# Kernel optimization log

Measured on AMD Instinct MI355X. Metric: run time of the kernel, lower is better.

## Reference

```python
import jax, jax.numpy as jnp
import numpy as np

DECAY = 0.99
EPS = 1e-5
COMMIT_COST = 0.25
VQ_COST = 1.0
COUNTER = 1  # first EMA step (hidden buffers are zero-initialized)


def setup_inputs() -> dict:
    key = jax.random.key(0)
    k1, k2 = jax.random.split(key)
    B, D, T, K = 64, 128, 2048, 1024
    x = jax.random.normal(k1, (B, D, T), dtype=jnp.float32)
    # xavier_uniform for [K, D]
    limit = float(np.sqrt(6.0 / (K + D)))
    embeddings = jax.random.uniform(k2, (K, D), minval=-limit, maxval=limit, dtype=jnp.float32)
    ema_dw_hidden = jnp.zeros((K, D), dtype=jnp.float32)
    ema_cluster_hidden = jnp.zeros((K,), dtype=jnp.float32)
    return {"x": x, "embeddings": embeddings,
            "ema_dw_hidden": ema_dw_hidden, "ema_cluster_hidden": ema_cluster_hidden}


def reference(x, embeddings, ema_dw_hidden, ema_cluster_hidden):
    K, D = embeddings.shape
    xt = jnp.transpose(x, (0, 2, 1))          # [B, T, D]
    flat = xt.reshape(-1, D)                  # [N, D]
    dist = (jnp.sum(flat * flat, axis=1, keepdims=True)
            + jnp.sum(embeddings * embeddings, axis=1)
            - 2.0 * flat @ embeddings.T)      # [N, K]
    idx = jnp.argmin(dist, axis=1)            # [N]
    quantized = embeddings[idx].reshape(xt.shape)  # [B, T, D]

    # --- EMA codebook update (no grad; pure stats) ---
    counts = jax.ops.segment_sum(jnp.ones_like(idx, dtype=jnp.float32), idx, num_segments=K)  # [K]
    hid_cs = ema_cluster_hidden - (ema_cluster_hidden - counts) * (1.0 - DECAY)
    avg_cs = hid_cs / (1.0 - DECAY ** COUNTER)
    n = jnp.sum(avg_cs)
    cs = (avg_cs + EPS) / (n + K * EPS) * n   # Laplace-smoothed cluster size
    dw = jax.ops.segment_sum(flat, idx, num_segments=K)  # [K, D] == encodings.T @ flat
    hid_dw = ema_dw_hidden - (ema_dw_hidden - dw) * (1.0 - DECAY)
    avg_dw = hid_dw / (1.0 - DECAY ** COUNTER)
    new_embeddings = avg_dw / cs[:, None]

    # --- losses + straight-through estimator ---
    sg = jax.lax.stop_gradient
    loss_commit = COMMIT_COST * jnp.mean((xt - sg(quantized)) ** 2)
    loss_vq = VQ_COST * jnp.mean((sg(xt) - quantized) ** 2)
    q_st = xt + sg(quantized - xt)
    out = jnp.transpose(q_st, (0, 2, 1))      # [B, D, T]
    return (out, loss_commit, loss_vq, idx, new_embeddings)
```

## Files before the change

### kernel.cpp

```cpp
#include <hip/hip_runtime.h>

#define NB 64
#define ND 128
#define NT 2048
#define NK 1024
#define NN (NB*NT)
#define DTSTRIDE (ND*NT)

typedef __attribute__((ext_vector_type(8))) short bf16x8;
typedef __attribute__((ext_vector_type(4))) float floatx4;

#define WS_ET    0
#define WS_SSX   131072
#define WS_SSE   262144
#define WS_DW    263168
#define WS_CS    394240
#define WS_CNT   395264
#define WS_IDX   396288
#define WS_LOSS  527360
#define WS_OFFS  527364
#define WS_CUR   528388
#define WS_LIST  529412
#define WS_XT    660736
#define WS_EB    17437952

#define O_OUT 0
#define O_LC  16777216
#define O_LV  16777217
#define O_IDX 16777218
#define O_NE  16908290

#define GLL16(g, l) __builtin_amdgcn_global_load_lds( \
    (const __attribute__((address_space(1))) unsigned int*)(g), \
    (__attribute__((address_space(3))) unsigned int*)(l), 16, 0, 0)

__device__ inline void split1(float v, unsigned short &a, unsigned short &b,
                              unsigned short &c) {
    unsigned int u = __float_as_uint(v);
    a = (unsigned short)(u >> 16);
    float f1 = __uint_as_float(u & 0xffff0000u);
    float r = v - f1;
    unsigned int ur = __float_as_uint(r);
    b = (unsigned short)(ur >> 16);
    float f2 = __uint_as_float(ur & 0xffff0000u);
    float r2 = r - f2;
    c = (unsigned short)(__float_as_uint(r2) >> 16);
}

__device__ inline void split2(float va, float vb, unsigned int &p1,
                              unsigned int &p2, unsigned int &p3) {
    unsigned int ua = __float_as_uint(va), ub = __float_as_uint(vb);
    p1 = (ua >> 16) | (ub & 0xffff0000u);
    float fa = __uint_as_float(ua & 0xffff0000u);
    float fb = __uint_as_float(ub & 0xffff0000u);
    float ra = va - fa, rb = vb - fb;
    unsigned int ura = __float_as_uint(ra), urb = __float_as_uint(rb);
    p2 = (ura >> 16) | (urb & 0xffff0000u);
    float f2a = __uint_as_float(ura & 0xffff0000u);
    float f2b = __uint_as_float(urb & 0xffff0000u);
    float r2a = ra - f2a, r2b = rb - f2b;
    p3 = (__float_as_uint(r2a) >> 16) | (__float_as_uint(r2b) & 0xffff0000u);
}

__global__ void prep_e(const float* __restrict__ emb, float* __restrict__ ET,
                       float* __restrict__ sse, unsigned short* __restrict__ eb1,
                       unsigned short* __restrict__ eb2, unsigned short* __restrict__ eb3) {
    int tid = threadIdx.x;
    int k   = blockIdx.x * 16 + (tid >> 4);
    int l   = tid & 15;
    float ss = 0.f;
    #pragma unroll
    for (int it = 0; it < 2; ++it) {
        int d0 = l * 4 + it * 64;
        float4 v = *(const float4*)(emb + k * ND + d0);
        ET[(d0+0)*NK + k] = v.x;
        ET[(d0+1)*NK + k] = v.y;
        ET[(d0+2)*NK + k] = v.z;
        ET[(d0+3)*NK + k] = v.w;
        ss = fmaf(v.x, v.x, ss); ss = fmaf(v.y, v.y, ss);
        ss = fmaf(v.z, v.z, ss); ss = fmaf(v.w, v.w, ss);
        int dc  = (l >> 3) + it * 2;
        int d5  = d0 & 31;
        int qb  = (d5 >> 3) & 3;
        int sl  = qb ^ ((k >> 1) & 3);
        int off = (dc * NK + k) * 32 + (sl << 3) + (d5 & 7);
        ushort4 a, b, c;
        split1(v.x, a.x, b.x, c.x);
        split1(v.y, a.y, b.y, c.y);
        split1(v.z, a.z, b.z, c.z);
        split1(v.w, a.w, b.w, c.w);
        *(ushort4*)(eb1 + off) = a;
        *(ushort4*)(eb2 + off) = b;
        *(ushort4*)(eb3 + off) = c;
    }
    for (int m = 1; m <= 8; m <<= 1) ss += __shfl_xor(ss, m);
    if (l == 0) sse[k] = ss;
}

__global__ void transpose_x(const float* __restrict__ x, float* __restrict__ xt,
                            float* __restrict__ ssx) {
    __shared__ float tile[128][33];
    int tid = threadIdx.x;
    int b   = blockIdx.x >> 6;
    int t0  = (blockIdx.x & 63) << 5;
    int tl  = tid & 31;
    int dg  = tid >> 5;
    const float* xp = x + b * DTSTRIDE + t0 + tl;
    #pragma unroll
    for (int p = 0; p < 16; ++p) {
        int d = p * 8 + dg;
        tile[d][tl] = xp[d * NT];
    }
    __syncthreads();
    float* xtp = xt + (size_t)(b * NT + t0) * ND;
    #pragma unroll
    for (int c = 0; c < 4; ++c) {
        int d = c * 32 + (tid & 31);
        #pragma unroll
        for (int p = 0; p < 4; ++p) {
            int tr = p * 8 + (tid >> 5);
            xtp[tr * ND + d] = tile[d][tr];
        }
    }
    if (tid < 32) {
        float ss = 0.f;
        #pragma unroll 8
        for (int d = 0; d < ND; ++d) {
            float v = tile[d][tid];
            ss = fmaf(v, v, ss);
        }
        ssx[b * NT + t0 + tid] = ss;
    }
}

__device__ __forceinline__ void stage_eb(int ktp, int dcp, int bufidx, int w, int lane,
        unsigned short* smem, const unsigned short* eb1,
        const unsigned short* eb2, const unsigned short* eb3) {
    int goff = (dcp << 15) + (ktp << 12);
    int bufo = bufidx * 12288;
    #pragma unroll
    for (int i = 0; i < 2; ++i) {
        int ch = (w << 1) + i;
        int so = goff + (ch << 9) + (lane << 3);
        GLL16(eb1 + so, &smem[bufo + 0*4096 + (ch << 9)]);
        GLL16(eb2 + so, &smem[bufo + 1*4096 + (ch << 9)]);
        GLL16(eb3 + so, &smem[bufo + 2*4096 + (ch << 9)]);
    }
}

__device__ __forceinline__ int m3(int v) { return v >= 3 ? v - 3 : v; }

__launch_bounds__(256, 2)
__global__ void gemm_argmin_mfma(const float* __restrict__ xt,
                                 const unsigned short* __restrict__ eb1,
                                 const unsigned short* __restrict__ eb2,
                                 const unsigned short* __restrict__ eb3,
                                 const float* __restrict__ ssx, const float* __restrict__ sse,
                                 float* __restrict__ out, int* __restrict__ idxi,
                                 int* __restrict__ counts, float* __restrict__ loss) {
    __shared__ unsigned short smem[38912];
    int tid = threadIdx.x;
    int b   = blockIdx.x >> 4;
    int t0  = (blockIdx.x & 15) << 7;
    int n0  = b * NT + t0;

    int lane = tid & 63;
    int w    = tid >> 6;
    int c    = lane & 15;
    int q    = lane >> 4;
    int slot = q ^ ((c >> 1) & 3);

    stage_eb(0, 0, 0, w, lane, smem, eb1, eb2, eb3);

    float* ssef = (float*)&smem[36864];
    ((float4*)ssef)[tid] = ((const float4*)sse)[tid];

    bf16x8 af[4][2][3];
    #pragma unroll
    for (int dc = 0; dc < 4; ++dc) {
        #pragma unroll
        for (int i = 0; i < 2; ++i) {
            const float* xp = xt + (size_t)(n0 + w*32 + i*16 + c) * ND + dc*32 + q*8;
            float4 v0 = *(const float4*)(xp + 0);
            float4 v1 = *(const float4*)(xp + 4);
            unsigned int p1[4], p2[4], p3[4];
            split2(v0.x, v0.y, p1[0], p2[0], p3[0]);
            split2(v0.z, v0.w, p1[1], p2[1], p3[1]);
            split2(v1.x, v1.y, p1[2], p2[2], p3[2]);
            split2(v1.z, v1.w, p1[3], p2[3], p3[3]);
            uint4 u;
            u = make_uint4(p1[0], p1[1], p1[2], p1[3]); af[dc][i][0] = *(bf16x8*)&u;
            u = make_uint4(p2[0], p2[1], p2[2], p2[3]); af[dc][i][1] = *(bf16x8*)&u;
            u = make_uint4(p3[0], p3[1], p3[2], p3[3]); af[dc][i][2] = *(bf16x8*)&u;
        }
    }

    float ssxv[8];
    #pragma unroll
    for (int i = 0; i < 2; ++i)
        #pragma unroll
        for (int rr = 0; rr < 4; ++rr)
            ssxv[i*4+rr] = ssx[n0 + w*32 + i*16 + q*4 + rr];

    stage_eb(0, 1, 1, w, lane, smem, eb1, eb2, eb3);

    float bestD[8]; int bestK[8];
    #pragma unroll
    for (int i = 0; i < 8; ++i) { bestD[i] = 3.4e38f; bestK[i] = 0; }

    floatx4 acc[2][8];
    int b3 = 0;

    for (int kt = 0; kt < 8; ++kt) {
        #pragma unroll
        for (int i = 0; i < 2; ++i)
            #pragma unroll
            for (int j = 0; j < 8; ++j)
                acc[i][j] = (floatx4){0.f, 0.f, 0.f, 0.f};

        #pragma unroll
        for (int dc = 0; dc < 4; ++dc) {
            int cur = (dc == 0 || dc == 3) ? b3 : m3(b3 + dc);

            if (kt == 7 && dc == 3) {
                asm volatile("s_waitcnt vmcnt(0) lgkmcnt(0)" ::: "memory");
            } else {
                asm volatile("s_waitcnt vmcnt(6) lgkmcnt(0)" ::: "memory");
            }
            __builtin_amdgcn_s_barrier();

            if (dc == 0) {
                stage_eb(kt, 2, m3(b3 + 2), w, lane, smem, eb1, eb2, eb3);
            } else if (dc == 1) {
                stage_eb(kt, 3, b3, w, lane, smem, eb1, eb2, eb3);
            } else if (dc == 2) {
                if (kt < 7) stage_eb(kt + 1, 0, m3(b3 + 1), w, lane, smem, eb1, eb2, eb3);
            } else {
                if (kt < 7) stage_eb(kt + 1, 1, m3(b3 + 2), w, lane, smem, eb1, eb2, eb3);
            }

            int bufo = cur * 12288;
            __builtin_amdgcn_s_setprio(1);
            #pragma unroll
            for (int j = 0; j < 8; ++j) {
                int ro = bufo + ((j << 4) + c) * 32 + slot * 8;
                bf16x8 b1 = *(const bf16x8*)(&smem[ro + 0*4096]);
                bf16x8 b2 = *(const bf16x8*)(&smem[ro + 1*4096]);
                bf16x8 b3f = *(const bf16x8*)(&smem[ro + 2*4096]);
                #pragma unroll
                for (int i = 0; i < 2; ++i) {
                    acc[i][j] = __builtin_amdgcn_mfma_f32_16x16x32_bf16(af[dc][i][0], b1, acc[i][j], 0, 0, 0);
                    acc[i][j] = __builtin_amdgcn_mfma_f32_16x16x32_bf16(af[dc][i][0], b2, acc[i][j], 0, 0, 0);
                    acc[i][j] = __builtin_amdgcn_mfma_f32_16x16x32_bf16(af[dc][i][1], b1, acc[i][j], 0, 0, 0);
                    acc[i][j] = __builtin_amdgcn_mfma_f32_16x16x32_bf16(af[dc][i][1], b2, acc[i][j], 0, 0, 0);
                    acc[i][j] = __builtin_amdgcn_mfma_f32_16x16x32_bf16(af[dc][i][0], b3f, acc[i][j], 0, 0, 0);
                    acc[i][j] = __builtin_amdgcn_mfma_f32_16x16x32_bf16(af[dc][i][2], b1, acc[i][j], 0, 0, 0);
                }
            }
            __builtin_amdgcn_s_setprio(0);
        }

        #pragma unroll
        for (int j = 0; j < 8; ++j) {
            int   kidx = (kt << 7) + (j << 4) + c;
            float se = ssef[(kt << 7) + (j << 4) + c];
            #pragma unroll
            for (int i = 0; i < 2; ++i) {
                #pragma unroll
                for (int rr = 0; rr < 4; ++rr) {
                    float t1   = ssxv[i*4+rr] + se;
                    float dist = fmaf(-2.f, acc[i][j][rr], t1);
                    if (dist < bestD[i*4+rr]) { bestD[i*4+rr] = dist; bestK[i*4+rr] = kidx; }
                }
            }
        }
        b3 = m3(b3 + 1);
    }

    #pragma unroll
    for (int i = 0; i < 8; ++i) {
        float d = bestD[i]; int kk = bestK[i];
        for (int m = 1; m <= 8; m <<= 1) {
            float od = __shfl_xor(d, m);
            int   ok = __shfl_xor(kk, m);
            if (od < d || (od == d && ok < kk)) { d = od; kk = ok; }
        }
        bestD[i] = d; bestK[i] = kk;
    }
    if (c == 0) {
        float ls = 0.f;
        #pragma unroll
        for (int i = 0; i < 2; ++i)
            #pragma unroll
            for (int rr = 0; rr < 4; ++rr) {
                int n = n0 + w*32 + i*16 + q*4 + rr;
                int kk = bestK[i*4+rr];
                out[O_IDX + n] = (float)kk;
                idxi[n] = kk;
                atomicAdd(&counts[kk], 1);
                ls += bestD[i*4+rr];
            }
        atomicAdd(loss, ls);
    }
}

__global__ void out_write(const float* __restrict__ x, const float* __restrict__ ET,
                          const int* __restrict__ idxi, float* __restrict__ out) {
    int b = blockIdx.x >> 3;
    int t = ((blockIdx.x & 7) << 8) + threadIdx.x;
    int k = idxi[b * NT + t];
    const float* xp = x + b * DTSTRIDE + t;
    float*       op = out + O_OUT + b * DTSTRIDE + t;
    #pragma unroll 4
    for (int d = 0; d < ND; ++d) {
        float xv = xp[d * NT];
        float q  = ET[d * NK + k];
        op[d * NT] = xv + (q - xv);
    }
}

__global__ void scan_cs(const int* __restrict__ counts, int* __restrict__ offs,
                        int* __restrict__ cur, const float* __restrict__ ch,
                        const float* __restrict__ loss, float* __restrict__ csv,
                        float* __restrict__ out) {
    __shared__ int   s[256];
    __shared__ float red[256];
    int tid = threadIdx.x;
    int c[4]; int sum = 0;
    #pragma unroll
    for (int j = 0; j < 4; ++j) { c[j] = counts[tid*4+j]; sum += c[j]; }
    s[tid] = sum; __syncthreads();
    for (int off = 1; off < 256; off <<= 1) {
        int v = (tid >= off) ? s[tid - off] : 0;
        __syncthreads();
        s[tid] += v;
        __syncthreads();
    }
    int base = (tid == 0) ? 0 : s[tid-1];
    #pragma unroll
    for (int j = 0; j < 4; ++j) {
        offs[tid*4+j] = base; cur[tid*4+j] = base; base += c[j];
    }
    __syncthreads();
    const float DECF = (float)(1.0 - 0.99);
    float sf = 0.f;
    #pragma unroll
    for (int rr = 0; rr < 4; ++rr) {
        int k = tid + rr * 256;
        float cc = (float)counts[k];
        float e = ch[k];
        float hid = e - (e - cc) * DECF;
        sf += hid / DECF;
    }
    red[tid] = sf; __syncthreads();
    for (int off = 128; off > 0; off >>= 1) {
        if (tid < off) red[tid] += red[tid + off];
        __syncthreads();
    }
    float n = red[0];
    const float KEPSF = (float)(1024.0 * 1e-5);
    #pragma unroll
    for (int rr = 0; rr < 4; ++rr) {
        int k = tid + rr * 256;
        float cc = (float)counts[k];
        float e = ch[k];
        float hid = e - (e - cc) * DECF;
        float a = hid / DECF;
        csv[k] = (a + 1e-5f) / (n + KEPSF) * n;
    }
    if (tid == 0) {
        float mean = loss[0] / 16777216.f;
        out[O_LC] = 0.25f * mean;
        out[O_LV] = mean;
    }
}

__global__ void fill_list(const int* __restrict__ idxi, int* __restrict__ cur,
                          int* __restrict__ list) {
    int n = blockIdx.x * 256 + threadIdx.x;
    int k = idxi[n];
    int pos = atomicAdd(&cur[k], 1);
    list[pos] = n;
}

__global__ void dw_sum(const float* __restrict__ xt,
                       const int* __restrict__ counts, const int* __restrict__ offs,
                       const int* __restrict__ list, float* __restrict__ dw) {
    __shared__ float red[128];
    int k = blockIdx.x;
    int d = threadIdx.x & 127;
    int h = threadIdx.x >> 7;
    int cnt = counts[k], base = offs[k];
    float acc = 0.f;
    for (int m = h; m < cnt; m += 2) {
        int n = list[base + m];
        acc += xt[(size_t)n * ND + d];
    }
    if (h == 1) red[d] = acc;
    __syncthreads();
    if (h == 0) dw[k * ND + d] = acc + red[d];
}

__global__ void new_emb(const float* __restrict__ dw, const float* __restrict__ dwh,
                        const float* __restrict__ csv, float* __restrict__ out) {
    int kd = blockIdx.x * 256 + threadIdx.x;
    const float DECF = (float)(1.0 - 0.99);
    float e = dwh[kd];
    float hid = e - (e - dw[kd]) * DECF;
    float a = hid / DECF;
    out[O_NE + kd] = a / csv[kd >> 7];
}

extern "C" void kernel_launch(void* const* d_in, const int* in_sizes, int n_in,
                              void* d_out, int out_size, void* d_ws, size_t ws_size,
                              hipStream_t stream) {
    const float* x   = (const float*)d_in[0];
    const float* emb = (const float*)d_in[1];
    const float* dwh = (const float*)d_in[2];
    const float* ch  = (const float*)d_in[3];
    float* out = (float*)d_out;
    float* ws  = (float*)d_ws;

    float* ET   = ws + WS_ET;
    float* ssx  = ws + WS_SSX;
    float* sse  = ws + WS_SSE;
    float* dw   = ws + WS_DW;
    float* csv  = ws + WS_CS;
    int*   counts = (int*)(ws + WS_CNT);
    int*   idxi   = (int*)(ws + WS_IDX);
    float* loss   = ws + WS_LOSS;
    int*   offs   = (int*)(ws + WS_OFFS);
    int*   cur    = (int*)(ws + WS_CUR);
    int*   list   = (int*)(ws + WS_LIST);
    float* xt     = ws + WS_XT;
    unsigned short* eb1 = (unsigned short*)(ws + WS_EB);
    unsigned short* eb2 = eb1 + NK * ND;
    unsigned short* eb3 = eb2 + NK * ND;

    hipMemsetAsync(counts, 0, NK * sizeof(int), stream);
    hipMemsetAsync(loss, 0, sizeof(float), stream);

    prep_e         <<<64,   256, 0, stream>>>(emb, ET, sse, eb1, eb2, eb3);
    transpose_x    <<<4096, 256, 0, stream>>>(x, xt, ssx);
    gemm_argmin_mfma<<<1024,256, 0, stream>>>(xt, eb1, eb2, eb3, ssx, sse, out, idxi, counts, loss);
    out_write      <<<512,  256, 0, stream>>>(x, ET, idxi, out);
    scan_cs        <<<1,    256, 0, stream>>>(counts, offs, cur, ch, loss, csv, out);
    fill_list      <<<512,  256, 0, stream>>>(idxi, cur, list);
    dw_sum         <<<1024, 256, 0, stream>>>(xt, counts, offs, list, dw);
    new_emb        <<<512,  256, 0, stream>>>(dw, dwh, csv, out);
}
```

Baseline: 436.0 us.

## Fuse output write into GEMM-argmin epilogue and EMA update into dw_sum

Each GEMM block now stores its winning indices in shared memory and writes the straight-through output for its 128 tokens itself, using the codebook gather from ET. This removes the separate out_write launch and its idx reload. The EMA new-embedding computation is folded into dw_sum, which removes the new_emb kernel and the dw round trip through memory. The cost is a longer GEMM tail, with extra strided global traffic on a kernel that runs two blocks per CU. Reusing smem for ksh after the main loop depends on all earlier smem reads having finished before the index writes.

```diff
diff --git a/kernel.cpp b/kernel.cpp
--- a/kernel.cpp
+++ b/kernel.cpp
@@ -156,6 +156,7 @@
                                  const unsigned short* __restrict__ eb2,
                                  const unsigned short* __restrict__ eb3,
                                  const float* __restrict__ ssx, const float* __restrict__ sse,
+                                 const float* __restrict__ x, const float* __restrict__ ET,
                                  float* __restrict__ out, int* __restrict__ idxi,
                                  int* __restrict__ counts, float* __restrict__ loss) {
     __shared__ unsigned short smem[38912];
@@ -287,35 +288,37 @@
         }
         bestD[i] = d; bestK[i] = kk;
     }
+    int* ksh = (int*)smem;
     if (c == 0) {
         float ls = 0.f;
         #pragma unroll
         for (int i = 0; i < 2; ++i)
             #pragma unroll
             for (int rr = 0; rr < 4; ++rr) {
-                int n = n0 + w*32 + i*16 + q*4 + rr;
+                int r  = w*32 + i*16 + q*4 + rr;
+                int n  = n0 + r;
                 int kk = bestK[i*4+rr];
                 out[O_IDX + n] = (float)kk;
                 idxi[n] = kk;
+                ksh[r] = kk;
                 atomicAdd(&counts[kk], 1);
                 ls += bestD[i*4+rr];
             }
         atomicAdd(loss, ls);
     }
-}
-
-__global__ void out_write(const float* __restrict__ x, const float* __restrict__ ET,
-                          const int* __restrict__ idxi, float* __restrict__ out) {
-    int b = blockIdx.x >> 3;
-    int t = ((blockIdx.x & 7) << 8) + threadIdx.x;
-    int k = idxi[b * NT + t];
-    const float* xp = x + b * DTSTRIDE + t;
-    float*       op = out + O_OUT + b * DTSTRIDE + t;
+    __syncthreads();
+
+    int tl2 = tid & 127;
+    int dh  = tid >> 7;
+    int kk2 = ksh[tl2];
+    const float* xp2 = x + b * DTSTRIDE + t0 + tl2;
+    float*       op2 = out + O_OUT + b * DTSTRIDE + t0 + tl2;
     #pragma unroll 4
-    for (int d = 0; d < ND; ++d) {
-        float xv = xp[d * NT];
-        float q  = ET[d * NK + k];
-        op[d * NT] = xv + (q - xv);
+    for (int s = 0; s < 64; ++s) {
+        int d = s * 2 + dh;
+        float xv = xp2[d * NT];
+        float qv = ET[d * NK + kk2];
+        op2[d * NT] = xv + (qv - xv);
     }
 }
 
@@ -385,7 +388,8 @@
 
 __global__ void dw_sum(const float* __restrict__ xt,
                        const int* __restrict__ counts, const int* __restrict__ offs,
-                       const int* __restrict__ list, float* __restrict__ dw) {
+                       const int* __restrict__ list, const float* __restrict__ dwh,
+                       const float* __restrict__ csv, float* __restrict__ out) {
     __shared__ float red[128];
     int k = blockIdx.x;
     int d = threadIdx.x & 127;
@@ -398,17 +402,15 @@
     }
     if (h == 1) red[d] = acc;
     __syncthreads();
-    if (h == 0) dw[k * ND + d] = acc + red[d];
-}
-
-__global__ void new_emb(const float* __restrict__ dw, const float* __restrict__ dwh,
-                        const float* __restrict__ csv, float* __restrict__ out) {
-    int kd = blockIdx.x * 256 + threadIdx.x;
-    const float DECF = (float)(1.0 - 0.99);
-    float e = dwh[kd];
-    float hid = e - (e - dw[kd]) * DECF;
-    float a = hid / DECF;
-    out[O_NE + kd] = a / csv[kd >> 7];
+    if (h == 0) {
+        const float DECF = (float)(1.0 - 0.99);
+        float dwv = acc + red[d];
+        int   kd  = k * ND + d;
+        float e   = dwh[kd];
+        float hid = e - (e - dwv) * DECF;
+        float a   = hid / DECF;
+        out[O_NE + kd] = a / csv[k];
+    }
 }
 
 extern "C" void kernel_launch(void* const* d_in, const int* in_sizes, int n_in,
@@ -424,7 +426,6 @@
     float* ET   = ws + WS_ET;
     float* ssx  = ws + WS_SSX;
     float* sse  = ws + WS_SSE;
-    float* dw   = ws + WS_DW;
     float* csv  = ws + WS_CS;
     int*   counts = (int*)(ws + WS_CNT);
     int*   idxi   = (int*)(ws + WS_IDX);
@@ -442,10 +443,9 @@
 
     prep_e         <<<64,   256, 0, stream>>>(emb, ET, sse, eb1, eb2, eb3);
     transpose_x    <<<4096, 256, 0, stream>>>(x, xt, ssx);
-    gemm_argmin_mfma<<<1024,256, 0, stream>>>(xt, eb1, eb2, eb3, ssx, sse, out, idxi, counts, loss);
-    out_write      <<<512,  256, 0, stream>>>(x, ET, idxi, out);
+    gemm_argmin_mfma<<<1024,256, 0, stream>>>(xt, eb1, eb2, eb3, ssx, sse, x, ET,
+                                              out, idxi, counts, loss);
     scan_cs        <<<1,    256, 0, stream>>>(counts, offs, cur, ch, loss, csv, out);
     fill_list      <<<512,  256, 0, stream>>>(idxi, cur, list);
-    dw_sum         <<<1024, 256, 0, stream>>>(xt, counts, offs, list, dw);
-    new_emb        <<<512,  256, 0, stream>>>(dw, dwh, csv, out);
-}
+    dw_sum         <<<1024, 256, 0, stream>>>(xt, counts, offs, list, dwh, csv, out);
+}
```

Result: faster. 424.4 us (-2.7%).
